# Kernel tuning notes

Hardware: AMD Instinct MI355X
Metric: run time of the kernel (lower is better)

The kernel has to match this reference:

```python
import jax, jax.numpy as jnp
import numpy as np

B, T, V, D, H, C = 128, 512, 50000, 128, 256, 10


def _lstm_scan(xs, W, U, b):
    # xs: [T, B, in]; Keras gate order i, f, g(candidate), o.
    xW = jnp.einsum('tbi,ij->tbj', xs, W) + b  # precompute input projection
    Bsz = xs.shape[1]
    Hd = U.shape[0]
    h0 = jnp.zeros((Bsz, Hd), xs.dtype)

    def step(carry, zx):
        h, c = carry
        z = zx + h @ U
        i, f, g, o = jnp.split(z, 4, axis=-1)
        i = jax.nn.sigmoid(i)
        f = jax.nn.sigmoid(f)
        g = jnp.tanh(g)
        o = jax.nn.sigmoid(o)
        c = f * c + i * g
        h = o * jnp.tanh(c)
        return (h, c), h

    (hT, _), hs = jax.lax.scan(step, (h0, h0), xW)
    return hs, hT


def setup_inputs() -> dict:
    key = jax.random.key(0)
    ks = jax.random.split(key, 16)
    f32 = jnp.float32

    def glorot(k, shape):
        fan = shape[0] + shape[1]
        return jax.random.uniform(k, shape, f32, -1.0, 1.0) * np.sqrt(6.0 / fan)

    x = jax.random.randint(ks[0], (B, T), 0, V, dtype=jnp.int32)
    emb = jax.random.normal(ks[1], (V, D), f32) * 0.05
    # layer 1: input D -> 4H per direction
    W1f = glorot(ks[2], (D, 4 * H)); U1f = glorot(ks[3], (H, 4 * H)); b1f = jnp.zeros((4 * H,), f32)
    W1b = glorot(ks[4], (D, 4 * H)); U1b = glorot(ks[5], (H, 4 * H)); b1b = jnp.zeros((4 * H,), f32)
    # layer 2: input 2H -> 4H per direction
    W2f = glorot(ks[6], (2 * H, 4 * H)); U2f = glorot(ks[7], (H, 4 * H)); b2f = jnp.zeros((4 * H,), f32)
    W2b = glorot(ks[8], (2 * H, 4 * H)); U2b = glorot(ks[9], (H, 4 * H)); b2b = jnp.zeros((4 * H,), f32)
    Wd = glorot(ks[10], (2 * H, C)); bd = jnp.zeros((C,), f32)
    return dict(x=x, emb=emb, W1f=W1f, U1f=U1f, b1f=b1f, W1b=W1b, U1b=U1b, b1b=b1b,
                W2f=W2f, U2f=U2f, b2f=b2f, W2b=W2b, U2b=U2b, b2b=b2b, Wd=Wd, bd=bd)


def reference(x, emb, W1f, U1f, b1f, W1b, U1b, b1b, W2f, U2f, b2f, W2b, U2b, b2b, Wd, bd):
    # Embedding lookup -> [T, B, D] (time-major for scan). Dropout is inference-off.
    e = jnp.transpose(emb[x], (1, 0, 2))
    # Bidirectional LSTM 1 (return_sequences)
    hs_f, _ = _lstm_scan(e, W1f, U1f, b1f)
    hs_b, _ = _lstm_scan(e[::-1], W1b, U1b, b1b)
    seq = jnp.concatenate([hs_f, hs_b[::-1]], axis=-1)  # [T, B, 2H]
    # Bidirectional LSTM 2 (return last states)
    _, hT_f = _lstm_scan(seq, W2f, U2f, b2f)
    _, hT_b = _lstm_scan(seq[::-1], W2b, U2b, b2b)
    h = jnp.concatenate([hT_f, hT_b], axis=-1)  # [B, 2H]
    return jax.nn.softmax(h @ Wd + bd, axis=-1)
```

## Files before the change

kernel.cpp:

```cpp
#include <hip/hip_runtime.h>
#include <hip/hip_bf16.h>

#define B_ 128
#define T_ 512
#define H_ 256
#define G4_ 1024
#define D_ 128

typedef short s8v   __attribute__((ext_vector_type(8)));
typedef float f32x4 __attribute__((ext_vector_type(4)));
typedef unsigned short u16x4 __attribute__((ext_vector_type(4)));
typedef unsigned short u16x8 __attribute__((ext_vector_type(8)));
typedef unsigned int   u32x4 __attribute__((ext_vector_type(4)));
typedef unsigned short ush;
typedef unsigned long long ull;

__device__ __align__(256) ush   g_xw[(size_t)T_ * 2 * B_ * G4_];
__device__ __align__(256) ush   g_hseq[(size_t)T_ * B_ * 512];
__device__ __align__(256) ull   g_hx2[16 * 2 * 2 * 256 * 4];
__device__ __align__(256) float g_hT[B_ * 512];
__device__ __align__(256) unsigned g_tcnt[512];
__device__ __align__(256) ush   g_wtall[2359296];

__device__ __forceinline__ ush f2b(float f) {
  unsigned u = __builtin_bit_cast(unsigned, f);
  u += 0x7FFFu + ((u >> 16) & 1u);
  return (ush)(u >> 16);
}
__device__ __forceinline__ float b2f(ush h) {
  unsigned u = ((unsigned)h) << 16;
  return __builtin_bit_cast(float, u);
}
__device__ __forceinline__ float sigm(float x) {
  x = fminf(15.f, fmaxf(-15.f, x));
  return 1.f / (1.f + __expf(-x));
}
__device__ __forceinline__ float tanh_(float x) {
  x = fminf(8.f, fmaxf(-8.f, x));
  float e = __expf(-2.f * x);
  return (1.f - e) / (1.f + e);
}

__global__ __launch_bounds__(256, 4) void prep_w(
    const float* __restrict__ Wf, const float* __restrict__ Wb,
    ush* __restrict__ WTf, ush* __restrict__ WTb, int K)
{
  __shared__ ush tile[64][65];
  const float* W = blockIdx.z ? Wb : Wf;
  ush* WT = blockIdx.z ? WTb : WTf;
  int nt = blockIdx.x & 15, kt = blockIdx.x >> 4;
  int tid = threadIdx.x;
  for (int i = tid; i < 4096; i += 256) {
    int k = i >> 6, n = i & 63;
    tile[k][n] = f2b(W[(size_t)(kt * 64 + k) * 1024 + nt * 64 + n]);
  }
  __syncthreads();
  for (int i = tid; i < 4096; i += 256) {
    int n = i >> 6, k = i & 63;
    WT[(size_t)(nt * 64 + n) * K + kt * 64 + k] = tile[k][n];
  }
}

__global__ __launch_bounds__(512, 4) void gemm_xw(
    const int* __restrict__ xi, const float* __restrict__ emb,
    const ush* __restrict__ WTf, const ush* __restrict__ WTb)
{
  __shared__ __align__(16) ush A_lds[128 * 72];
  __shared__ __align__(16) ush BT_lds[128 * 72];
  const int tid = threadIdx.x;
  const int lane = tid & 63;
  const int w = tid >> 6;
  const int nb = blockIdx.x;
  const int t = blockIdx.y;
  const int dir = blockIdx.z;
  const ush* WT = dir ? WTb : WTf;

  const f32x4 zero4 = {0.f, 0.f, 0.f, 0.f};
  f32x4 acc[8];
#pragma unroll
  for (int i = 0; i < 8; ++i) acc[i] = zero4;

  const int rowA0 = tid >> 3;
  const int ccA = tid & 7;
  int idx0 = xi[rowA0 * T_ + t];
  int idx1 = xi[(rowA0 + 64) * T_ + t];

  for (int kc = 0; kc < 2; ++kc) {
    __syncthreads();
    {
      const float* s = emb + (size_t)idx0 * D_ + kc * 64 + ccA * 8;
      f32x4 a = *(const f32x4*)s;
      f32x4 b = *(const f32x4*)(s + 4);
      u16x8 v;
      v[0]=f2b(a[0]); v[1]=f2b(a[1]); v[2]=f2b(a[2]); v[3]=f2b(a[3]);
      v[4]=f2b(b[0]); v[5]=f2b(b[1]); v[6]=f2b(b[2]); v[7]=f2b(b[3]);
      *(u16x8*)&A_lds[rowA0 * 72 + ccA * 8] = v;
    }
    {
      const float* s = emb + (size_t)idx1 * D_ + kc * 64 + ccA * 8;
      f32x4 a = *(const f32x4*)s;
      f32x4 b = *(const f32x4*)(s + 4);
      u16x8 v;
      v[0]=f2b(a[0]); v[1]=f2b(a[1]); v[2]=f2b(a[2]); v[3]=f2b(a[3]);
      v[4]=f2b(b[0]); v[5]=f2b(b[1]); v[6]=f2b(b[2]); v[7]=f2b(b[3]);
      *(u16x8*)&A_lds[(rowA0 + 64) * 72 + ccA * 8] = v;
    }
    {
      int n = tid >> 2, k8 = (tid & 3) * 2;
      const ush* src = WT + (size_t)(nb * 128 + n) * 128 + kc * 64 + k8 * 8;
      *(u32x4*)&BT_lds[n * 72 + k8 * 8] = *(const u32x4*)src;
      *(u32x4*)&BT_lds[n * 72 + k8 * 8 + 8] = *(const u32x4*)(src + 8);
    }
    __syncthreads();
#pragma unroll
    for (int kt = 0; kt < 2; ++kt) {
      const int koff = kt * 32 + ((lane >> 4) << 3);
      s8v af = *(const s8v*)&A_lds[(w * 16 + (lane & 15)) * 72 + koff];
#pragma unroll
      for (int nt = 0; nt < 8; ++nt) {
        s8v bf = *(const s8v*)&BT_lds[(nt * 16 + (lane & 15)) * 72 + koff];
        acc[nt] = __builtin_amdgcn_mfma_f32_16x16x32_bf16(af, bf, acc[nt], 0, 0, 0);
      }
    }
  }
  ush* dst = g_xw + ((size_t)t * 2 + dir) * ((size_t)B_ * G4_);
#pragma unroll
  for (int nt = 0; nt < 8; ++nt) {
    int colg = nb * 128 + nt * 16 + (lane & 15);
    int g = colg >> 8, hc = colg & 255;
#pragma unroll
    for (int jj = 0; jj < 4; ++jj) {
      int row = w * 16 + ((lane >> 4) << 2) + jj;
      dst[(size_t)row * 1024 + hc * 4 + g] = f2b(acc[nt][jj]);
    }
  }
}

__global__ __launch_bounds__(512, 2) void mega(
    int layer, const ush* __restrict__ UTf, const ush* __restrict__ UTb,
    const float* __restrict__ bfp, const float* __restrict__ bbp,
    int writeSeq, int ngemm,
    const ush* __restrict__ WT2f, const ush* __restrict__ WT2b)
{
  __shared__ __align__(16) ush smem[2 * 128 * 72];
  const int bx = blockIdx.x;
  const int tid = threadIdx.x;
  const int lane = tid & 63;
  const int w = tid >> 6;
  const int l15 = lane & 15;
  const int lq = lane >> 4;

  if (bx < 64) {
    const int slice = bx & 15;
    const int dir = (bx >> 4) & 1;
    const int nh = bx >> 5;
    const ush* UT = dir ? UTb : UTf;
    const float* bias = dir ? bbp : bfp;
    const int mycol = nh * 128 + w * 16 + l15;
    const int rowb = slice * 8;
    const unsigned sbase = (unsigned)(layer * T_);
    ush* h0 = smem;

    s8v bfr[4][8];
#pragma unroll
    for (int g = 0; g < 4; ++g) {
      const ush* up = UT + (size_t)(g * 256 + mycol) * 256;
#pragma unroll
      for (int kt = 0; kt < 8; ++kt)
        bfr[g][kt] = *(const s8v*)(up + kt * 32 + lq * 8);
    }
    float bias_r[4];
#pragma unroll
    for (int g = 0; g < 4; ++g) bias_r[g] = bias[g * 256 + mycol];

    {
      ull* z = (ull*)smem;
      z[tid] = 0ull; z[tid + 512] = 0ull; z[tid + 1024] = 0ull; z[tid + 1536] = 0ull;
    }
    __syncthreads();

    float c_[4] = {0.f, 0.f, 0.f, 0.f};
    ull* hx_base = g_hx2 + (size_t)(slice * 2 + dir) * 2048;
    const int colp = (nh ^ 1) * 128 + (tid >> 2);
    const int m_ = tid & 3;
    const int c8p = colp >> 3, wp = colp & 7;
    const int xrow = (lq & 1) * 4;

    u16x4 xv[4];
    {
      int t0 = dir ? (T_ - 1) : 0;
      const ush* xp = g_xw + (((size_t)t0 * 2 + dir) * B_ + rowb) * 1024 + mycol * 4;
#pragma unroll
      for (int j = 0; j < 4; ++j) xv[j] = *(const u16x4*)(xp + (size_t)(xrow + j) * 1024);
    }

    for (int s = 0; s < T_; ++s) {
      const int p = s & 1;
      if (s > 0) {
        ull* aP = hx_base + ((size_t)p * 256 + colp) * 4 + m_;
        unsigned target = sbase + (unsigned)s;
        ull v;
        for (;;) {
          v = __hip_atomic_load(aP, __ATOMIC_RELAXED, __HIP_MEMORY_SCOPE_SYSTEM);
          if ((unsigned)(v >> 32) >= target) break;
          __builtin_amdgcn_s_sleep(1);
        }
        int r0 = 2 * m_;
        ush* dl = h0 + p * 4096;
        dl[r0 * 256 + (((c8p ^ r0) & 31) * 8 + wp)] = (ush)v;
        dl[(r0 + 1) * 256 + (((c8p ^ (r0 + 1)) & 31) * 8 + wp)] = (ush)(v >> 16);
      }
      __syncthreads();
      if (writeSeq) {
        if (tid == 0 && s >= 2) {
          int td = dir ? (T_ + 1 - s) : (s - 2);
          __hip_atomic_fetch_add(&g_tcnt[td], 1u, __ATOMIC_RELAXED, __HIP_MEMORY_SCOPE_SYSTEM);
        }
        if (s > 0 && tid < 128) {
          int row8 = tid >> 4, idx = tid & 15;
          int col = nh * 128 + idx * 8;
          int c8 = col >> 3;
          const ush* srcl = h0 + p * 4096 + row8 * 256 + ((c8 ^ row8) & 31) * 8;
          ull lo = *(const ull*)srcl;
          ull hi = *(const ull*)(srcl + 4);
          int tprev = dir ? (T_ - s) : (s - 1);
          ull* dst = (ull*)&g_hseq[((size_t)tprev * B_ + rowb + row8) * 512 + dir * 256 + col];
          __hip_atomic_store(dst, lo, __ATOMIC_RELAXED, __HIP_MEMORY_SCOPE_SYSTEM);
          __hip_atomic_store(dst + 1, hi, __ATOMIC_RELAXED, __HIP_MEMORY_SCOPE_SYSTEM);
        }
      }
      u16x4 xn[4];
      if (s + 1 < T_) {
        int tn = dir ? (T_ - 2 - s) : (s + 1);
        const ush* xp = g_xw + (((size_t)tn * 2 + dir) * B_ + rowb) * 1024 + mycol * 4;
#pragma unroll
        for (int j = 0; j < 4; ++j) xn[j] = *(const u16x4*)(xp + (size_t)(xrow + j) * 1024);
      }
      s8v af[8];
#pragma unroll
      for (int kt = 0; kt < 8; ++kt) {
        int c8 = kt * 4 + lq;
        af[kt] = *(const s8v*)(h0 + p * 4096 + l15 * 256 + ((c8 ^ l15) & 31) * 8);
      }
      f32x4 acc[4];
      const f32x4 zero4 = {0.f, 0.f, 0.f, 0.f};
#pragma unroll
      for (int g = 0; g < 4; ++g) acc[g] = zero4;
#pragma unroll
      for (int kt = 0; kt < 8; ++kt) {
#pragma unroll
        for (int g = 0; g < 4; ++g)
          acc[g] = __builtin_amdgcn_mfma_f32_16x16x32_bf16(af[kt], bfr[g][kt], acc[g], 0, 0, 0);
      }
      float hf[4];
      ush hv[4];
#pragma unroll
      for (int j = 0; j < 4; ++j) {
        float vi = acc[0][j] + b2f(xv[j][0]) + bias_r[0];
        float vf = acc[1][j] + b2f(xv[j][1]) + bias_r[1];
        float vg = acc[2][j] + b2f(xv[j][2]) + bias_r[2];
        float vo = acc[3][j] + b2f(xv[j][3]) + bias_r[3];
        float ig = sigm(vi), fg = sigm(vf), gg = tanh_(vg), og = sigm(vo);
        float cc = fg * c_[j] + ig * gg;
        c_[j] = cc;
        hf[j] = og * tanh_(cc);
        hv[j] = f2b(hf[j]);
      }
      (void)hf;
      if (lq < 2) {
        ull seqw = ((ull)(sbase + (unsigned)s + 1u)) << 32;
        ull e0 = (ull)hv[0] | ((ull)hv[1] << 16) | seqw;
        ull e1 = (ull)hv[2] | ((ull)hv[3] << 16) | seqw;
        ull* ep = hx_base + ((size_t)(p ^ 1) * 256 + mycol) * 4 + 2 * lq;
        __hip_atomic_store(ep, e0, __ATOMIC_RELAXED, __HIP_MEMORY_SCOPE_SYSTEM);
        __hip_atomic_store(ep + 1, e1, __ATOMIC_RELAXED, __HIP_MEMORY_SCOPE_SYSTEM);
        int c8o = mycol >> 3, wo = mycol & 7;
        ush* dl = h0 + (p ^ 1) * 4096;
#pragma unroll
        for (int j = 0; j < 4; ++j) {
          int r = lq * 4 + j;
          dl[r * 256 + (((c8o ^ r) & 31) * 8 + wo)] = hv[j];
        }
      }
#pragma unroll
      for (int j = 0; j < 4; ++j) xv[j] = xn[j];
    }
    __syncthreads();
    const ush* bufl = h0 + (T_ & 1) * 4096;
    if (writeSeq) {
      if (tid < 128) {
        int row8 = tid >> 4, idx = tid & 15;
        int col = nh * 128 + idx * 8;
        int c8 = col >> 3;
        const ush* srcl = bufl + row8 * 256 + ((c8 ^ row8) & 31) * 8;
        ull lo = *(const ull*)srcl;
        ull hi = *(const ull*)(srcl + 4);
        int tlast = dir ? 0 : (T_ - 1);
        ull* dst = (ull*)&g_hseq[((size_t)tlast * B_ + rowb + row8) * 512 + dir * 256 + col];
        __hip_atomic_store(dst, lo, __ATOMIC_RELAXED, __HIP_MEMORY_SCOPE_SYSTEM);
        __hip_atomic_store(dst + 1, hi, __ATOMIC_RELAXED, __HIP_MEMORY_SCOPE_SYSTEM);
      }
      asm volatile("s_waitcnt vmcnt(0)" ::: "memory");
      __syncthreads();
      if (tid == 0) {
        int ta = dir ? 1 : (T_ - 2);
        int tb2 = dir ? 0 : (T_ - 1);
        __hip_atomic_fetch_add(&g_tcnt[ta], 1u, __ATOMIC_RELAXED, __HIP_MEMORY_SCOPE_SYSTEM);
        __hip_atomic_fetch_add(&g_tcnt[tb2], 1u, __ATOMIC_RELAXED, __HIP_MEMORY_SCOPE_SYSTEM);
      }
    } else {
      if (tid < 128) {
        int row8 = tid >> 4, idx = tid & 15;
        int col = nh * 128 + idx * 8;
        int c8 = col >> 3;
        const ush* srcl = bufl + row8 * 256 + ((c8 ^ row8) & 31) * 8;
        float* dstf = g_hT + (size_t)(rowb + row8) * 512 + dir * 256 + col;
        f32x4 f0, f1;
#pragma unroll
        for (int j = 0; j < 4; ++j) { f0[j] = b2f(srcl[j]); f1[j] = b2f(srcl[4 + j]); }
        *(f32x4*)dstf = f0;
        *(f32x4*)(dstf + 4) = f1;
      }
    }
  } else {
    if (ngemm <= 0) return;
    ush* A_lds = smem;
    ush* BT_lds = smem + 128 * 72;
    const int wg = bx - 64;
    const int rowA0 = tid >> 3;
    const int ccA = tid & 7;

    for (int u = wg; u < 8192; u += ngemm) {
      int pairIdx = u >> 4, sub = u & 15;
      int nb = sub & 7, gdir = sub >> 3;
      int t = (pairIdx & 1) ? (255 - (pairIdx >> 1)) : (256 + (pairIdx >> 1));
      const ush* WT = gdir ? WT2b : WT2f;
      for (;;) {
        unsigned v = __hip_atomic_load(&g_tcnt[t], __ATOMIC_RELAXED, __HIP_MEMORY_SCOPE_SYSTEM);
        if (v >= 64u) break;
        __builtin_amdgcn_s_sleep(4);
      }
      const f32x4 zero4 = {0.f, 0.f, 0.f, 0.f};
      f32x4 acc[8];
#pragma unroll
      for (int i = 0; i < 8; ++i) acc[i] = zero4;
      for (int kc = 0; kc < 8; ++kc) {
        __syncthreads();
        {
          const ush* s0 = g_hseq + ((size_t)(t * B_ + rowA0)) * 512 + kc * 64 + ccA * 8;
          *(u32x4*)&A_lds[rowA0 * 72 + ccA * 8] = *(const u32x4*)s0;
          const ush* s1 = g_hseq + ((size_t)(t * B_ + rowA0 + 64)) * 512 + kc * 64 + ccA * 8;
          *(u32x4*)&A_lds[(rowA0 + 64) * 72 + ccA * 8] = *(const u32x4*)s1;
        }
        {
          int n = tid >> 2, k8 = (tid & 3) * 2;
          const ush* src = WT + (size_t)(nb * 128 + n) * 512 + kc * 64 + k8 * 8;
          *(u32x4*)&BT_lds[n * 72 + k8 * 8] = *(const u32x4*)src;
          *(u32x4*)&BT_lds[n * 72 + k8 * 8 + 8] = *(const u32x4*)(src + 8);
        }
        __syncthreads();
#pragma unroll
        for (int kt = 0; kt < 2; ++kt) {
          const int koff = kt * 32 + (lq << 3);
          s8v af = *(const s8v*)&A_lds[(w * 16 + l15) * 72 + koff];
#pragma unroll
          for (int nt = 0; nt < 8; ++nt) {
            s8v bf = *(const s8v*)&BT_lds[(nt * 16 + l15) * 72 + koff];
            acc[nt] = __builtin_amdgcn_mfma_f32_16x16x32_bf16(af, bf, acc[nt], 0, 0, 0);
          }
        }
      }
      ush* dst = g_xw + ((size_t)t * 2 + gdir) * ((size_t)B_ * G4_);
#pragma unroll
      for (int nt = 0; nt < 8; ++nt) {
        int colg = nb * 128 + nt * 16 + l15;
        int g = colg >> 8, hc = colg & 255;
#pragma unroll
        for (int jj = 0; jj < 4; ++jj) {
          int row = w * 16 + (lq << 2) + jj;
          dst[(size_t)row * 1024 + hc * 4 + g] = f2b(acc[nt][jj]);
        }
      }
    }
  }
}

__global__ __launch_bounds__(512, 1) void dense_softmax(
    const float* __restrict__ Wd, const float* __restrict__ bd, float* __restrict__ out)
{
  __shared__ float wT[10 * 512];
  __shared__ float part[512 * 10];
  int tid = threadIdx.x;
  for (int i = tid; i < 5120; i += 512) {
    int k = i / 10, j = i - k * 10;
    wT[j * 512 + k] = Wd[i];
  }
  __syncthreads();
  int row = tid >> 2, q = tid & 3;
  float acc[10];
#pragma unroll
  for (int j = 0; j < 10; ++j) acc[j] = 0.f;
  const float* hrow = g_hT + (size_t)row * 512 + q * 128;
  for (int kk = 0; kk < 32; ++kk) {
    f32x4 h4 = *(const f32x4*)(hrow + kk * 4);
#pragma unroll
    for (int j = 0; j < 10; ++j) {
      f32x4 w4 = *(const f32x4*)&wT[j * 512 + q * 128 + kk * 4];
      acc[j] += h4[0] * w4[0] + h4[1] * w4[1] + h4[2] * w4[2] + h4[3] * w4[3];
    }
  }
#pragma unroll
  for (int j = 0; j < 10; ++j) part[tid * 10 + j] = acc[j];
  __syncthreads();
  if (tid < 128) {
    float lg[10];
#pragma unroll
    for (int j = 0; j < 10; ++j)
      lg[j] = bd[j] + part[(tid * 4 + 0) * 10 + j] + part[(tid * 4 + 1) * 10 + j]
                    + part[(tid * 4 + 2) * 10 + j] + part[(tid * 4 + 3) * 10 + j];
    float m = lg[0];
#pragma unroll
    for (int j = 1; j < 10; ++j) m = fmaxf(m, lg[j]);
    float ssum = 0.f;
#pragma unroll
    for (int j = 0; j < 10; ++j) { lg[j] = __expf(lg[j] - m); ssum += lg[j]; }
    float inv = 1.f / ssum;
#pragma unroll
    for (int j = 0; j < 10; ++j) out[tid * 10 + j] = lg[j] * inv;
  }
}

extern "C" void kernel_launch(void* const* d_in, const int* in_sizes, int n_in,
                              void* d_out, int out_size, void* d_ws, size_t ws_size,
                              hipStream_t stream) {
  (void)in_sizes; (void)n_in; (void)d_ws; (void)ws_size; (void)out_size;
  const int* x = (const int*)d_in[0];
  const float* emb = (const float*)d_in[1];
  const float* W1f = (const float*)d_in[2];
  const float* U1f = (const float*)d_in[3];
  const float* b1f = (const float*)d_in[4];
  const float* W1b = (const float*)d_in[5];
  const float* U1b = (const float*)d_in[6];
  const float* b1b = (const float*)d_in[7];
  const float* W2f = (const float*)d_in[8];
  const float* U2f = (const float*)d_in[9];
  const float* b2f = (const float*)d_in[10];
  const float* W2b = (const float*)d_in[11];
  const float* U2b = (const float*)d_in[12];
  const float* b2b = (const float*)d_in[13];
  const float* Wd  = (const float*)d_in[14];
  const float* bd  = (const float*)d_in[15];
  float* out = (float*)d_out;

  void* hx_p = nullptr; void* wt_p = nullptr; void* tc_p = nullptr;
  hipGetSymbolAddress(&hx_p, HIP_SYMBOL(g_hx2));
  hipGetSymbolAddress(&wt_p, HIP_SYMBOL(g_wtall));
  hipGetSymbolAddress(&tc_p, HIP_SYMBOL(g_tcnt));
  ush* wt = (ush*)wt_p;
  hipMemsetAsync(hx_p, 0, sizeof(ull) * 16 * 2 * 2 * 256 * 4, stream);
  hipMemsetAsync(tc_p, 0, sizeof(unsigned) * 512, stream);

  ush* wt1f = wt;                 ush* wt1b = wt1f + 131072;
  ush* ut1f = wt1b + 131072;      ush* ut1b = ut1f + 262144;
  ush* wt2f = ut1b + 262144;      ush* wt2b = wt2f + 524288;
  ush* ut2f = wt2b + 524288;      ush* ut2b = ut2f + 262144;

  prep_w<<<dim3(32, 1, 2), 256, 0, stream>>>(W1f, W1b, wt1f, wt1b, 128);
  prep_w<<<dim3(64, 1, 2), 256, 0, stream>>>(U1f, U1b, ut1f, ut1b, 256);
  prep_w<<<dim3(128, 1, 2), 256, 0, stream>>>(W2f, W2b, wt2f, wt2b, 512);
  prep_w<<<dim3(64, 1, 2), 256, 0, stream>>>(U2f, U2b, ut2f, ut2b, 256);

  gemm_xw<<<dim3(8, T_, 2), 512, 0, stream>>>(x, emb, wt1f, wt1b);
  mega<<<224, 512, 0, stream>>>(0, ut1f, ut1b, b1f, b1b, 1, 160, wt2f, wt2b);
  mega<<<64, 512, 0, stream>>>(1, ut2f, ut2b, b2f, b2b, 0, 0, nullptr, nullptr);
  dense_softmax<<<1, 512, 0, stream>>>(Wd, bd, out);
}
```

Baseline: 3.788 ms.

## Split recurrent matmul into local and remote halves to overlap cross-block exchange

Each block now computes the half of the h@U product that uses its own freshly produced hidden columns right after writing them, before waiting for the partner block's half. Only the remote half is computed after the spin-wait, which shortens the serial critical path per timestep. The hidden-state exchange buffer is relaid out so each thread polls one coalesced slot, and __syncthreads is replaced with a lightweight LDS-wait barrier. The grid for layer 1 grows from 224 to 256 blocks with more GEMM-helper blocks. This risks ordering bugs from the weaker barrier and the changed exchange layout.

New measurement: 10.07 ms. +165.7%, slower.

```diff
diff --git a/kernel.cpp b/kernel.cpp
--- a/kernel.cpp
+++ b/kernel.cpp
@@ -15,9 +15,11 @@
 typedef unsigned short ush;
 typedef unsigned long long ull;
 
+#define BAR_LDS() asm volatile("s_waitcnt lgkmcnt(0)\n\ts_barrier" ::: "memory")
+
 __device__ __align__(256) ush   g_xw[(size_t)T_ * 2 * B_ * G4_];
 __device__ __align__(256) ush   g_hseq[(size_t)T_ * B_ * 512];
-__device__ __align__(256) ull   g_hx2[16 * 2 * 2 * 256 * 4];
+__device__ __align__(256) ull   g_hx2[16 * 2 * 2 * 2 * 512];
 __device__ __align__(256) float g_hT[B_ * 512];
 __device__ __align__(256) unsigned g_tcnt[512];
 __device__ __align__(256) ush   g_wtall[2359296];
@@ -180,11 +182,18 @@
     __syncthreads();
 
     float c_[4] = {0.f, 0.f, 0.f, 0.f};
-    ull* hx_base = g_hx2 + (size_t)(slice * 2 + dir) * 2048;
-    const int colp = (nh ^ 1) * 128 + (tid >> 2);
-    const int m_ = tid & 3;
-    const int c8p = colp >> 3, wp = colp & 7;
+    ull* hx_sd = g_hx2 + (size_t)(slice * 2 + dir) * 2048;
+
+    const int w_src = tid >> 6, r_ = tid & 63;
+    const int blkc = r_ >> 5, lqs = (r_ >> 4) & 1, l15s = r_ & 15;
+    const int col_p = (nh ^ 1) * 128 + w_src * 16 + l15s;
+    const int r0c = lqs * 4 + blkc * 2;
+    const int c8p = col_p >> 3, wp = col_p & 7;
+    const int sw0 = ((c8p ^ r0c) & 31) * 8 + wp;
+    const int sw1 = ((c8p ^ (r0c + 1)) & 31) * 8 + wp;
     const int xrow = (lq & 1) * 4;
+    const int kto = nh * 4;
+    const int ktp = (nh ^ 1) * 4;
 
     u16x4 xv[4];
     {
@@ -194,23 +203,27 @@
       for (int j = 0; j < 4; ++j) xv[j] = *(const u16x4*)(xp + (size_t)(xrow + j) * 1024);
     }
 
+    const f32x4 zero4 = {0.f, 0.f, 0.f, 0.f};
+    f32x4 acc[4];
+#pragma unroll
+    for (int g = 0; g < 4; ++g) acc[g] = zero4;
+
     for (int s = 0; s < T_; ++s) {
       const int p = s & 1;
       if (s > 0) {
-        ull* aP = hx_base + ((size_t)p * 256 + colp) * 4 + m_;
+        const ull* ap = hx_sd + (size_t)(p * 2 + (nh ^ 1)) * 512 + tid;
         unsigned target = sbase + (unsigned)s;
         ull v;
         for (;;) {
-          v = __hip_atomic_load(aP, __ATOMIC_RELAXED, __HIP_MEMORY_SCOPE_SYSTEM);
+          v = __hip_atomic_load(ap, __ATOMIC_RELAXED, __HIP_MEMORY_SCOPE_SYSTEM);
           if ((unsigned)(v >> 32) >= target) break;
           __builtin_amdgcn_s_sleep(1);
         }
-        int r0 = 2 * m_;
         ush* dl = h0 + p * 4096;
-        dl[r0 * 256 + (((c8p ^ r0) & 31) * 8 + wp)] = (ush)v;
-        dl[(r0 + 1) * 256 + (((c8p ^ (r0 + 1)) & 31) * 8 + wp)] = (ush)(v >> 16);
-      }
-      __syncthreads();
+        dl[r0c * 256 + sw0] = (ush)v;
+        dl[(r0c + 1) * 256 + sw1] = (ush)(v >> 16);
+      }
+      BAR_LDS();
       if (writeSeq) {
         if (tid == 0 && s >= 2) {
           int td = dir ? (T_ + 1 - s) : (s - 2);
@@ -230,29 +243,21 @@
         }
       }
       u16x4 xn[4];
-      if (s + 1 < T_) {
-        int tn = dir ? (T_ - 2 - s) : (s + 1);
+      {
+        int tn = dir ? max(0, T_ - 2 - s) : min(T_ - 1, s + 1);
         const ush* xp = g_xw + (((size_t)tn * 2 + dir) * B_ + rowb) * 1024 + mycol * 4;
 #pragma unroll
         for (int j = 0; j < 4; ++j) xn[j] = *(const u16x4*)(xp + (size_t)(xrow + j) * 1024);
       }
-      s8v af[8];
-#pragma unroll
-      for (int kt = 0; kt < 8; ++kt) {
+#pragma unroll
+      for (int i = 0; i < 4; ++i) {
+        int kt = ktp + i;
         int c8 = kt * 4 + lq;
-        af[kt] = *(const s8v*)(h0 + p * 4096 + l15 * 256 + ((c8 ^ l15) & 31) * 8);
-      }
-      f32x4 acc[4];
-      const f32x4 zero4 = {0.f, 0.f, 0.f, 0.f};
-#pragma unroll
-      for (int g = 0; g < 4; ++g) acc[g] = zero4;
-#pragma unroll
-      for (int kt = 0; kt < 8; ++kt) {
+        s8v af = *(const s8v*)(h0 + p * 4096 + l15 * 256 + ((c8 ^ l15) & 31) * 8);
 #pragma unroll
         for (int g = 0; g < 4; ++g)
-          acc[g] = __builtin_amdgcn_mfma_f32_16x16x32_bf16(af[kt], bfr[g][kt], acc[g], 0, 0, 0);
-      }
-      float hf[4];
+          acc[g] = __builtin_amdgcn_mfma_f32_16x16x32_bf16(af, bfr[g][kt], acc[g], 0, 0, 0);
+      }
       ush hv[4];
 #pragma unroll
       for (int j = 0; j < 4; ++j) {
@@ -263,17 +268,18 @@
         float ig = sigm(vi), fg = sigm(vf), gg = tanh_(vg), og = sigm(vo);
         float cc = fg * c_[j] + ig * gg;
         c_[j] = cc;
-        hf[j] = og * tanh_(cc);
-        hv[j] = f2b(hf[j]);
-      }
-      (void)hf;
-      if (lq < 2) {
+        hv[j] = f2b(og * tanh_(cc));
+      }
+      asm volatile("" ::: "memory");
+      if (lq < 2 && s + 1 < T_) {
         ull seqw = ((ull)(sbase + (unsigned)s + 1u)) << 32;
         ull e0 = (ull)hv[0] | ((ull)hv[1] << 16) | seqw;
         ull e1 = (ull)hv[2] | ((ull)hv[3] << 16) | seqw;
-        ull* ep = hx_base + ((size_t)(p ^ 1) * 256 + mycol) * 4 + 2 * lq;
+        ull* ep = hx_sd + (size_t)((p ^ 1) * 2 + nh) * 512 + w * 64 + lq * 16 + l15;
         __hip_atomic_store(ep, e0, __ATOMIC_RELAXED, __HIP_MEMORY_SCOPE_SYSTEM);
-        __hip_atomic_store(ep + 1, e1, __ATOMIC_RELAXED, __HIP_MEMORY_SCOPE_SYSTEM);
+        __hip_atomic_store(ep + 32, e1, __ATOMIC_RELAXED, __HIP_MEMORY_SCOPE_SYSTEM);
+      }
+      if (lq < 2) {
         int c8o = mycol >> 3, wo = mycol & 7;
         ush* dl = h0 + (p ^ 1) * 4096;
 #pragma unroll
@@ -282,10 +288,21 @@
           dl[r * 256 + (((c8o ^ r) & 31) * 8 + wo)] = hv[j];
         }
       }
+      BAR_LDS();
+#pragma unroll
+      for (int g = 0; g < 4; ++g) acc[g] = zero4;
+#pragma unroll
+      for (int i = 0; i < 4; ++i) {
+        int kt = kto + i;
+        int c8 = kt * 4 + lq;
+        s8v af = *(const s8v*)(h0 + (p ^ 1) * 4096 + l15 * 256 + ((c8 ^ l15) & 31) * 8);
+#pragma unroll
+        for (int g = 0; g < 4; ++g)
+          acc[g] = __builtin_amdgcn_mfma_f32_16x16x32_bf16(af, bfr[g][kt], acc[g], 0, 0, 0);
+      }
 #pragma unroll
       for (int j = 0; j < 4; ++j) xv[j] = xn[j];
     }
-    __syncthreads();
     const ush* bufl = h0 + (T_ & 1) * 4096;
     if (writeSeq) {
       if (tid < 128) {
@@ -457,7 +474,7 @@
   hipGetSymbolAddress(&wt_p, HIP_SYMBOL(g_wtall));
   hipGetSymbolAddress(&tc_p, HIP_SYMBOL(g_tcnt));
   ush* wt = (ush*)wt_p;
-  hipMemsetAsync(hx_p, 0, sizeof(ull) * 16 * 2 * 2 * 256 * 4, stream);
+  hipMemsetAsync(hx_p, 0, sizeof(ull) * 16 * 2 * 2 * 2 * 512, stream);
   hipMemsetAsync(tc_p, 0, sizeof(unsigned) * 512, stream);
 
   ush* wt1f = wt;                 ush* wt1b = wt1f + 131072;
@@ -471,7 +488,7 @@
   prep_w<<<dim3(64, 1, 2), 256, 0, stream>>>(U2f, U2b, ut2f, ut2b, 256);
 
   gemm_xw<<<dim3(8, T_, 2), 512, 0, stream>>>(x, emb, wt1f, wt1b);
-  mega<<<224, 512, 0, stream>>>(0, ut1f, ut1b, b1f, b1b, 1, 160, wt2f, wt2b);
+  mega<<<256, 512, 0, stream>>>(0, ut1f, ut1b, b1f, b1b, 1, 192, wt2f, wt2b);
   mega<<<64, 512, 0, stream>>>(1, ut2f, ut2b, b2f, b2b, 0, 0, nullptr, nullptr);
   dense_softmax<<<1, 512, 0, stream>>>(Wd, bd, out);
 }
```
